# Performance work log

Hardware: AMD Instinct MI355X
Metric: run time of the kernel (lower is better)

The kernel has to match this reference:

```python
import jax, jax.numpy as jnp
import numpy as np

B, N, D, H, DH, FF, L, K, V = 16, 512, 512, 8, 64, 2048, 4, 16, 10000

def _ln(x, g, b, eps=1e-5):
    mu = jnp.mean(x, axis=-1, keepdims=True)
    var = jnp.var(x, axis=-1, keepdims=True)
    return (x - mu) * jax.lax.rsqrt(var + eps) * g + b

def setup_inputs() -> dict:
    key = jax.random.key(0)
    ks = jax.random.split(key, 24)
    s = lambda i, shape, sc=0.02: jax.random.normal(ks[i], shape, dtype=jnp.float32) * sc
    return {
        'node_ids': jax.random.randint(ks[0], (B * N,), 0, V, dtype=jnp.int32),
        'eigvecs': jax.random.normal(ks[1], (B * N, K), dtype=jnp.float32),
        'adj': jax.random.bernoulli(ks[2], 0.1, (B, N, N)),
        'emb': s(3, (V, D), 1.0),
        'pe_w': s(4, (K, D)), 'pe_b': jnp.zeros((D,), jnp.float32),
        'wq': s(5, (L, D, D)), 'bq': jnp.zeros((L, D), jnp.float32),
        'wk': s(6, (L, D, D)), 'bk': jnp.zeros((L, D), jnp.float32),
        'wv': s(7, (L, D, D)), 'bv': jnp.zeros((L, D), jnp.float32),
        'wo': s(8, (L, D, D)), 'bo': jnp.zeros((L, D), jnp.float32),
        'ln1_g': jnp.ones((L, D), jnp.float32), 'ln1_b': jnp.zeros((L, D), jnp.float32),
        'ln2_g': jnp.ones((L, D), jnp.float32), 'ln2_b': jnp.zeros((L, D), jnp.float32),
        'w1': s(9, (L, D, FF)), 'b1': jnp.zeros((L, FF), jnp.float32),
        'w2': s(10, (L, FF, D)), 'b2': jnp.zeros((L, D), jnp.float32),
    }

def reference(node_ids, eigvecs, adj, emb, pe_w, pe_b, wq, bq, wk, bk, wv, bv, wo, bo,
              ln1_g, ln1_b, ln2_g, ln2_b, w1, b1, w2, b2):
    # embedding + Laplacian PE (dropout = identity at eval)
    h = emb[node_ids] + eigvecs @ pe_w + pe_b          # [B*N, D]
    x = h.reshape(B, N, D)                              # dense batch (equal graph sizes)
    # faithful to torch _canonical_mask: -inf WHERE bool mask is True
    mask = jnp.where(adj, -jnp.inf, 0.0)[:, None, :, :]  # [B,1,N,N] broadcast over heads
    scale = 1.0 / jnp.sqrt(jnp.float32(DH))
    for i in range(L):
        q = (x @ wq[i] + bq[i]).reshape(B, N, H, DH)
        k = (x @ wk[i] + bk[i]).reshape(B, N, H, DH)
        v = (x @ wv[i] + bv[i]).reshape(B, N, H, DH)
        scores = jnp.einsum('bqhd,bkhd->bhqk', q, k) * scale + mask
        attn = jax.nn.softmax(scores, axis=-1)
        o = jnp.einsum('bhqk,bkhd->bqhd', attn, v).reshape(B, N, D)
        x = _ln(x + o @ wo[i] + bo[i], ln1_g[i], ln1_b[i])
        ff = jax.nn.relu(x @ w1[i] + b1[i]) @ w2[i] + b2[i]
        x = _ln(x + ff, ln2_g[i], ln2_b[i])
    return x.reshape(B * N, D)  # from_dense_batch with equal graph sizes
```

## Files before the change

### kernel.cpp

```cpp
#include <hip/hip_runtime.h>
#include <math.h>

#define NBATCH 16
#define NSEQ   512
#define DMODEL 512
#define NHEAD  8
#define DHEAD  64
#define FFDIM  2048
#define NLAYER 4
#define MROWS  (NBATCH * NSEQ)

typedef __attribute__((ext_vector_type(8))) short  short8v;
typedef __attribute__((ext_vector_type(4))) float  float4v;
typedef __attribute__((ext_vector_type(4))) unsigned short ushort4v;

__device__ __forceinline__ unsigned short f2bf(float x) {
    unsigned int u = __float_as_uint(x);
    u += 0x7FFFu + ((u >> 16) & 1u);
    return (unsigned short)(u >> 16);
}

__device__ __forceinline__ int xcd_chunk_orig(int bid, int nwg) {
    int q = nwg >> 3;
    return (bid & 7) * q + (bid >> 3);
}

__global__ void zero_flag_kernel(int* flag) {
    if (threadIdx.x == 0 && blockIdx.x == 0) flag[0] = 0;
}
__global__ void detect_adj_kernel(const unsigned char* __restrict__ a, int nbytes,
                                  int* __restrict__ flag) {
    int t = blockIdx.x * blockDim.x + threadIdx.x;
    int i = t * 4 + 1;
    int f = (i < nbytes) && (a[i] != 0);
    if (__any(f)) {
        if ((threadIdx.x & 63) == 0) atomicOr(flag, 1);
    }
}

__global__ __launch_bounds__(256) void build_mask_kernel(
        const void* __restrict__ adjp, const int* __restrict__ flag,
        unsigned long long* __restrict__ Mask) {
    int gw = (blockIdx.x * 256 + threadIdx.x) >> 6;
    int lane = threadIdx.x & 63;
    int nz;
    if (flag[0]) nz = ((const unsigned char*)adjp)[(size_t)gw * 64 + lane] != 0;
    else         nz = ((const int*)adjp)[(size_t)gw * 64 + lane] != 0;
    unsigned long long m = __ballot(nz);
    if (lane == 0) Mask[gw] = m;
}

__global__ __launch_bounds__(256) void transpose_cvt_kernel(
        const float* __restrict__ W, unsigned short* __restrict__ Wt,
        int K, int N, size_t in_stride, size_t out_stride, int row_off) {
    __shared__ float tile[32][33];
    const float* Wl = W + blockIdx.z * in_stride;
    unsigned short* Wo = Wt + blockIdx.z * out_stride;
    int n0 = blockIdx.x * 32, k0 = blockIdx.y * 32;
    int t = threadIdx.x;
    int r = t >> 3, c4 = (t & 7) * 4;
    float4 v = *(const float4*)(Wl + (size_t)(k0 + r) * N + n0 + c4);
    tile[r][c4 + 0] = v.x; tile[r][c4 + 1] = v.y;
    tile[r][c4 + 2] = v.z; tile[r][c4 + 3] = v.w;
    __syncthreads();
    ushort4v o;
    o.x = f2bf(tile[c4 + 0][r]); o.y = f2bf(tile[c4 + 1][r]);
    o.z = f2bf(tile[c4 + 2][r]); o.w = f2bf(tile[c4 + 3][r]);
    *(ushort4v*)(Wo + (size_t)(row_off + n0 + r) * K + k0 + c4) = o;
}

__global__ __launch_bounds__(256) void embed_kernel(
        const int* __restrict__ node_ids, const float* __restrict__ eigvecs,
        const float* __restrict__ emb, const float* __restrict__ pe_w,
        const float* __restrict__ pe_b, float* __restrict__ X,
        unsigned short* __restrict__ Xb) {
    int i = blockIdx.x * 256 + threadIdx.x;
    int row = i >> 9, d = i & 511;
    float acc = emb[(size_t)node_ids[row] * DMODEL + d] + pe_b[d];
    const float* ev = eigvecs + row * 16;
#pragma unroll
    for (int k = 0; k < 16; ++k) acc = fmaf(ev[k], pe_w[k * DMODEL + d], acc);
    X[i] = acc;
    Xb[i] = f2bf(acc);
}

template<int BN, int EPI>
__global__ __launch_bounds__(256) void bgemm_kernel(
        const unsigned short* __restrict__ A, const unsigned short* __restrict__ Bt,
        const float* __restrict__ bias0, const float* __restrict__ bias1,
        const float* __restrict__ bias2, const float* __restrict__ res,
        float* __restrict__ Cf, unsigned short* __restrict__ Cb0,
        unsigned short* __restrict__ Cb1, unsigned short* __restrict__ Cb2,
        int K, int N) {
    constexpr int WM = (BN == 128) ? 2 : 4;
    constexpr int WN = (BN == 128) ? 2 : 1;
    constexpr int MR = 128 / (WM * 16);
    constexpr int NR = BN / (WN * 16);
    __shared__ unsigned short Al[128 * 40];
    __shared__ unsigned short Bl[BN * 40];
    int tid = threadIdx.x;
    int nbn = N / BN;
    int orig = xcd_chunk_orig(blockIdx.x, gridDim.x);
    int bm = orig / nbn;
    int bn = orig - bm * nbn;
    int wid = tid >> 6, lane = tid & 63;
    int wr = wid / WN, wc = wid % WN;
    int l15 = lane & 15, lg = lane >> 4;
    float4v acc[MR][NR];
#pragma unroll
    for (int i = 0; i < MR; ++i)
#pragma unroll
        for (int j = 0; j < NR; ++j) { acc[i][j].x = 0.f; acc[i][j].y = 0.f; acc[i][j].z = 0.f; acc[i][j].w = 0.f; }
    const unsigned short* Ag = A + (size_t)(bm * 128) * K;
    const unsigned short* Bg = Bt + (size_t)(bn * BN) * K;
    for (int k0 = 0; k0 < K; k0 += 32) {
#pragma unroll
        for (int it = 0; it < 2; ++it) {
            int ch = tid + it * 256;
            int row = ch >> 2, c = ch & 3;
            *(short8v*)(Al + row * 40 + c * 8) =
                *(const short8v*)(Ag + (size_t)row * K + k0 + c * 8);
        }
#pragma unroll
        for (int it = 0; it < (BN == 128 ? 2 : 1); ++it) {
            int ch = tid + it * 256;
            int row = ch >> 2, c = ch & 3;
            *(short8v*)(Bl + row * 40 + c * 8) =
                *(const short8v*)(Bg + (size_t)row * K + k0 + c * 8);
        }
        __syncthreads();
        short8v af[MR], bf[NR];
#pragma unroll
        for (int rm = 0; rm < MR; ++rm)
            af[rm] = *(const short8v*)(Al + (wr * MR * 16 + rm * 16 + l15) * 40 + lg * 8);
#pragma unroll
        for (int cn = 0; cn < NR; ++cn)
            bf[cn] = *(const short8v*)(Bl + (wc * NR * 16 + cn * 16 + l15) * 40 + lg * 8);
#pragma unroll
        for (int rm = 0; rm < MR; ++rm)
#pragma unroll
            for (int cn = 0; cn < NR; ++cn)
                acc[rm][cn] = __builtin_amdgcn_mfma_f32_16x16x32_bf16(
                    af[rm], bf[cn], acc[rm][cn], 0, 0, 0);
        __syncthreads();
    }
#pragma unroll
    for (int cn = 0; cn < NR; ++cn) {
        int col = bn * BN + wc * NR * 16 + cn * 16 + l15;
        int seg = col >> 9, cs = col & 511;
        const float* bp = (EPI == 3) ? (seg == 0 ? bias0 : (seg == 1 ? bias1 : bias2)) : bias0;
        unsigned short* op = (EPI == 3) ? (seg == 0 ? Cb0 : (seg == 1 ? Cb1 : Cb2)) : Cb0;
        float bv = bp[(EPI == 3) ? cs : col];
#pragma unroll
        for (int rm = 0; rm < MR; ++rm) {
#pragma unroll
            for (int j = 0; j < 4; ++j) {
                int row = bm * 128 + wr * MR * 16 + rm * 16 + lg * 4 + j;
                float v = acc[rm][cn][j] + bv;
                if (EPI == 1) {
                    v += res[(size_t)row * N + col];
                    Cf[(size_t)row * N + col] = v;
                } else if (EPI == 2) {
                    op[(size_t)row * N + col] = f2bf(fmaxf(v, 0.f));
                } else {
                    op[(size_t)row * 512 + cs] = f2bf(v);
                }
            }
        }
    }
}

__global__ __launch_bounds__(256) void mattn_kernel(
        const unsigned short* __restrict__ Q, const unsigned short* __restrict__ Kb,
        const unsigned short* __restrict__ Vb,
        const unsigned long long* __restrict__ Mask,
        unsigned short* __restrict__ O) {
    __shared__ unsigned short Kl[64 * 72];
    __shared__ unsigned short Vt[64 * 72];
    __shared__ unsigned short Pl[4 * 16 * 72];
    __shared__ unsigned long long Ml[64 * 8];
    int tid = threadIdx.x;
    int bid = xcd_chunk_orig(blockIdx.x, gridDim.x);
    int qb = bid & 7, h = (bid >> 3) & 7, b = bid >> 6;
    int w = tid >> 6, lane = tid & 63, l15 = lane & 15, lg = lane >> 4;
    int q0 = qb * 64 + w * 16;

    {
        int base = (b * NSEQ + qb * 64) * 8;
        for (int it = tid; it < 512; it += 256) Ml[it] = Mask[base + it];
    }
    short8v qf[2];
    {
        const unsigned short* qp = Q + (size_t)(b * NSEQ + q0 + l15) * DMODEL + h * DHEAD + lg * 8;
        qf[0] = *(const short8v*)(qp);
        qf[1] = *(const short8v*)(qp + 32);
    }
    float m[4], lsum[4];
    float4v ao[4];
#pragma unroll
    for (int j = 0; j < 4; ++j) { m[j] = -1e30f; lsum[j] = 0.f; }
#pragma unroll
    for (int cn = 0; cn < 4; ++cn) { ao[cn].x = 0.f; ao[cn].y = 0.f; ao[cn].z = 0.f; ao[cn].w = 0.f; }

    for (int kt = 0; kt < 8; ++kt) {
        int kb0 = kt * 64;
        __syncthreads();
#pragma unroll
        for (int it = 0; it < 2; ++it) {
            int ch = tid + it * 256;
            int row = ch >> 3, c = ch & 7;
            short8v v = *(const short8v*)(Kb + (size_t)(b * NSEQ + kb0 + row) * DMODEL + h * DHEAD + c * 8);
            *(short8v*)(Kl + row * 72 + c * 8) = v;
        }
#pragma unroll
        for (int it = 0; it < 2; ++it) {
            int eb = tid + it * 256;
            int kj = eb & 63, d8 = eb >> 6;
            short8v v = *(const short8v*)(Vb + (size_t)(b * NSEQ + kb0 + kj) * DMODEL + h * DHEAD + d8 * 8);
#pragma unroll
            for (int e = 0; e < 8; ++e)
                Vt[(d8 * 8 + e) * 72 + kj] = (unsigned short)((short*)&v)[e];
        }
        __syncthreads();
        float4v sf[4];
#pragma unroll
        for (int kf = 0; kf < 4; ++kf) {
            short8v k0f = *(const short8v*)(Kl + (kf * 16 + l15) * 72 + lg * 8);
            short8v k1f = *(const short8v*)(Kl + (kf * 16 + l15) * 72 + 32 + lg * 8);
            float4v z; z.x = 0.f; z.y = 0.f; z.z = 0.f; z.w = 0.f;
            z = __builtin_amdgcn_mfma_f32_16x16x32_bf16(qf[0], k0f, z, 0, 0, 0);
            sf[kf] = __builtin_amdgcn_mfma_f32_16x16x32_bf16(qf[1], k1f, z, 0, 0, 0);
        }
        float sv[4][4];
#pragma unroll
        for (int j = 0; j < 4; ++j) {
            unsigned long long wm = Ml[(w * 16 + lg * 4 + j) * 8 + kt];
#pragma unroll
            for (int kf = 0; kf < 4; ++kf) {
                int bit = (int)((wm >> (kf * 16 + l15)) & 1ull);
                sv[kf][j] = sf[kf][j] * 0.125f + (bit ? -1e30f : 0.f);
            }
        }
#pragma unroll
        for (int j = 0; j < 4; ++j) {
            float t = sv[0][j];
#pragma unroll
            for (int kf = 1; kf < 4; ++kf) t = fmaxf(t, sv[kf][j]);
#pragma unroll
            for (int o = 1; o < 16; o <<= 1) t = fmaxf(t, __shfl_xor(t, o));
            float mn = fmaxf(m[j], t);
            float sc = exp2f((m[j] - mn) * 1.44269504f);
            float ps = 0.f;
            int prow = w * 16 + lg * 4 + j;
#pragma unroll
            for (int kf = 0; kf < 4; ++kf) {
                float p = exp2f((sv[kf][j] - mn) * 1.44269504f);
                Pl[prow * 72 + kf * 16 + l15] = f2bf(p);
                ps += p;
            }
#pragma unroll
            for (int o = 1; o < 16; o <<= 1) ps += __shfl_xor(ps, o);
            lsum[j] = lsum[j] * sc + ps;
            m[j] = mn;
#pragma unroll
            for (int cn = 0; cn < 4; ++cn) ao[cn][j] *= sc;
        }
#pragma unroll
        for (int s4 = 0; s4 < 2; ++s4) {
            short8v pa = *(const short8v*)(Pl + (w * 16 + l15) * 72 + s4 * 32 + lg * 8);
#pragma unroll
            for (int cn = 0; cn < 4; ++cn) {
                short8v vbf = *(const short8v*)(Vt + (cn * 16 + l15) * 72 + s4 * 32 + lg * 8);
                ao[cn] = __builtin_amdgcn_mfma_f32_16x16x32_bf16(pa, vbf, ao[cn], 0, 0, 0);
            }
        }
    }
#pragma unroll
    for (int j = 0; j < 4; ++j) lsum[j] = 1.f / lsum[j];
#pragma unroll
    for (int cn = 0; cn < 4; ++cn) {
        int d = cn * 16 + l15;
#pragma unroll
        for (int j = 0; j < 4; ++j) {
            int q = q0 + lg * 4 + j;
            O[(size_t)(b * NSEQ + q) * DMODEL + h * DHEAD + d] = f2bf(ao[cn][j] * lsum[j]);
        }
    }
}

__global__ __launch_bounds__(64) void ln_kernel(
        const float* __restrict__ Xin, const float* __restrict__ g,
        const float* __restrict__ be, float* __restrict__ Y,
        unsigned short* __restrict__ Yb) {
    int row = blockIdx.x;
    int t = threadIdx.x;
    const float* xr = Xin + (size_t)row * DMODEL;
    float4 a = *(const float4*)(xr + (t << 2));
    float4 c = *(const float4*)(xr + 256 + (t << 2));
    float s  = a.x + a.y + a.z + a.w + c.x + c.y + c.z + c.w;
    float ss = a.x*a.x + a.y*a.y + a.z*a.z + a.w*a.w
             + c.x*c.x + c.y*c.y + c.z*c.z + c.w*c.w;
#pragma unroll
    for (int o = 32; o; o >>= 1) { s += __shfl_xor(s, o); ss += __shfl_xor(ss, o); }
    float mu  = s * (1.f / 512.f);
    float var = ss * (1.f / 512.f) - mu * mu;
    float rinv = rsqrtf(var + 1e-5f);
    float4 g0 = *(const float4*)(g + (t << 2));
    float4 g1 = *(const float4*)(g + 256 + (t << 2));
    float4 b0 = *(const float4*)(be + (t << 2));
    float4 b1 = *(const float4*)(be + 256 + (t << 2));
    float4 o0, o1;
    o0.x = (a.x - mu) * rinv * g0.x + b0.x;
    o0.y = (a.y - mu) * rinv * g0.y + b0.y;
    o0.z = (a.z - mu) * rinv * g0.z + b0.z;
    o0.w = (a.w - mu) * rinv * g0.w + b0.w;
    o1.x = (c.x - mu) * rinv * g1.x + b1.x;
    o1.y = (c.y - mu) * rinv * g1.y + b1.y;
    o1.z = (c.z - mu) * rinv * g1.z + b1.z;
    o1.w = (c.w - mu) * rinv * g1.w + b1.w;
    *(float4*)(Y + (size_t)row * DMODEL + (t << 2)) = o0;
    *(float4*)(Y + (size_t)row * DMODEL + 256 + (t << 2)) = o1;
    if (Yb) {
        ushort4v u0, u1;
        u0.x = f2bf(o0.x); u0.y = f2bf(o0.y); u0.z = f2bf(o0.z); u0.w = f2bf(o0.w);
        u1.x = f2bf(o1.x); u1.y = f2bf(o1.y); u1.z = f2bf(o1.z); u1.w = f2bf(o1.w);
        *(ushort4v*)(Yb + (size_t)row * DMODEL + (t << 2)) = u0;
        *(ushort4v*)(Yb + (size_t)row * DMODEL + 256 + (t << 2)) = u1;
    }
}

extern "C" void kernel_launch(void* const* d_in, const int* in_sizes, int n_in,
                              void* d_out, int out_size, void* d_ws, size_t ws_size,
                              hipStream_t stream) {
    const int*   node_ids = (const int*)d_in[0];
    const float* eigvecs  = (const float*)d_in[1];
    const void*  adj      = d_in[2];
    const float* emb      = (const float*)d_in[3];
    const float* pe_w     = (const float*)d_in[4];
    const float* pe_b     = (const float*)d_in[5];
    const float* wq = (const float*)d_in[6];
    const float* bq = (const float*)d_in[7];
    const float* wk = (const float*)d_in[8];
    const float* bk = (const float*)d_in[9];
    const float* wv = (const float*)d_in[10];
    const float* bv = (const float*)d_in[11];
    const float* wo = (const float*)d_in[12];
    const float* bo = (const float*)d_in[13];
    const float* ln1_g = (const float*)d_in[14];
    const float* ln1_b = (const float*)d_in[15];
    const float* ln2_g = (const float*)d_in[16];
    const float* ln2_b = (const float*)d_in[17];
    const float* w1 = (const float*)d_in[18];
    const float* b1 = (const float*)d_in[19];
    const float* w2 = (const float*)d_in[20];
    const float* b2 = (const float*)d_in[21];
    float* out = (float*)d_out;

    const size_t MB = 1024ull * 1024ull;
    char* ws = (char*)d_ws;
    float*          X  = (float*)(ws + 0 * MB);
    float*          T  = (float*)(ws + 16 * MB);
    unsigned short* Xb = (unsigned short*)(ws + 32 * MB);
    unsigned short* Qb = (unsigned short*)(ws + 40 * MB);
    unsigned short* Kc = (unsigned short*)(ws + 48 * MB);
    unsigned short* Vc = (unsigned short*)(ws + 56 * MB);
    unsigned short* Ob = (unsigned short*)(ws + 64 * MB);
    unsigned short* Fb = (unsigned short*)(ws + 72 * MB);
    unsigned short* wqkvt = (unsigned short*)(ws + 104 * MB);
    unsigned short* wot   = (unsigned short*)(ws + 110 * MB);
    unsigned short* w1t   = (unsigned short*)(ws + 112 * MB);
    unsigned short* w2t   = (unsigned short*)(ws + 120 * MB);
    unsigned long long* Mask = (unsigned long long*)(ws + 128 * MB);
    int*            flag = (int*)(ws + 129 * MB);
    if (ws_size < 130 * MB) return;

    const size_t DD = (size_t)DMODEL * DMODEL;
    const size_t DF = (size_t)DMODEL * FFDIM;
    const size_t QKV = (size_t)3 * DD;

    zero_flag_kernel<<<1, 64, 0, stream>>>(flag);
    detect_adj_kernel<<<4096, 256, 0, stream>>>((const unsigned char*)adj,
                                                NBATCH * NSEQ * NSEQ, flag);
    build_mask_kernel<<<(MROWS * 8 * 64) / 256, 256, 0, stream>>>(adj, flag, Mask);
    {
        dim3 gdd(DMODEL / 32, DMODEL / 32, NLAYER);
        transpose_cvt_kernel<<<gdd, 256, 0, stream>>>(wq, wqkvt, DMODEL, DMODEL, DD, QKV, 0);
        transpose_cvt_kernel<<<gdd, 256, 0, stream>>>(wk, wqkvt, DMODEL, DMODEL, DD, QKV, 512);
        transpose_cvt_kernel<<<gdd, 256, 0, stream>>>(wv, wqkvt, DMODEL, DMODEL, DD, QKV, 1024);
        transpose_cvt_kernel<<<gdd, 256, 0, stream>>>(wo, wot, DMODEL, DMODEL, DD, DD, 0);
        dim3 g1t(FFDIM / 32, DMODEL / 32, NLAYER);
        transpose_cvt_kernel<<<g1t, 256, 0, stream>>>(w1, w1t, DMODEL, FFDIM, DF, DF, 0);
        dim3 g2t(DMODEL / 32, FFDIM / 32, NLAYER);
        transpose_cvt_kernel<<<g2t, 256, 0, stream>>>(w2, w2t, FFDIM, DMODEL, DF, DF, 0);
    }
    embed_kernel<<<(MROWS * DMODEL) / 256, 256, 0, stream>>>(node_ids, eigvecs, emb,
                                                             pe_w, pe_b, X, Xb);
    const int gQKV = (1536 / 128) * (MROWS / 128);
    const int gF   = (FFDIM / 128) * (MROWS / 128);
    const int gO   = (DMODEL / 64) * (MROWS / 128);
    const int gA   = NBATCH * NHEAD * (NSEQ / 64);
    for (int i = 0; i < NLAYER; ++i) {
        bgemm_kernel<128, 3><<<gQKV, 256, 0, stream>>>(
            Xb, wqkvt + i * QKV, bq + i * DMODEL, bk + i * DMODEL, bv + i * DMODEL,
            nullptr, nullptr, Qb, Kc, Vc, DMODEL, 1536);
        mattn_kernel<<<gA, 256, 0, stream>>>(
            Qb, Kc, Vc, Mask, Ob);
        bgemm_kernel<64, 1><<<gO, 256, 0, stream>>>(
            Ob, wot + i * DD, bo + i * DMODEL, nullptr, nullptr,
            X, T, nullptr, nullptr, nullptr, DMODEL, DMODEL);
        ln_kernel<<<MROWS, 64, 0, stream>>>(T, ln1_g + i * DMODEL, ln1_b + i * DMODEL, X, Xb);
        bgemm_kernel<128, 2><<<gF, 256, 0, stream>>>(
            Xb, w1t + i * DF, b1 + i * FFDIM, nullptr, nullptr,
            nullptr, nullptr, Fb, nullptr, nullptr, DMODEL, FFDIM);
        bgemm_kernel<64, 1><<<gO, 256, 0, stream>>>(
            Fb, w2t + i * DF, b2 + i * DMODEL, nullptr, nullptr,
            X, T, nullptr, nullptr, nullptr, FFDIM, DMODEL);
        int last = (i == NLAYER - 1);
        ln_kernel<<<MROWS, 64, 0, stream>>>(T, ln2_g + i * DMODEL, ln2_b + i * DMODEL,
                                            last ? out : X, last ? nullptr : Xb);
    }
}
```

Measured before the change: 899.2 us.

## Double-buffer GEMM tiles using direct global-to-LDS loads

The bf16 GEMM kernel now stages its A and B tiles with global_load_lds, which writes straight into LDS without passing through registers. It also uses two LDS buffers so the next K-slice is fetched while the current one feeds the MFMAs. The goal is to hide global memory latency and cut register traffic in the main loop. The unpadded 32-element row stride can cause LDS bank conflicts on the fragment reads. Correctness depends on the loop's synchronisation also waiting for the asynchronous LDS writes to finish.

```diff
diff --git a/kernel.cpp b/kernel.cpp
--- a/kernel.cpp
+++ b/kernel.cpp
@@ -18,6 +18,12 @@
     unsigned int u = __float_as_uint(x);
     u += 0x7FFFu + ((u >> 16) & 1u);
     return (unsigned short)(u >> 16);
+}
+
+__device__ __forceinline__ void gload16(const unsigned short* g, unsigned short* l) {
+    __builtin_amdgcn_global_load_lds(
+        (const __attribute__((address_space(1))) unsigned int*)g,
+        (__attribute__((address_space(3))) unsigned int*)l, 16, 0, 0);
 }
 
 __device__ __forceinline__ int xcd_chunk_orig(int bid, int nwg) {
@@ -96,8 +102,9 @@
     constexpr int WN = (BN == 128) ? 2 : 1;
     constexpr int MR = 128 / (WM * 16);
     constexpr int NR = BN / (WN * 16);
-    __shared__ unsigned short Al[128 * 40];
-    __shared__ unsigned short Bl[BN * 40];
+    constexpr int BCH = BN / 64;
+    __shared__ unsigned short Al[2][128 * 32];
+    __shared__ unsigned short Bl[2][BN * 32];
     int tid = threadIdx.x;
     int nbn = N / BN;
     int orig = xcd_chunk_orig(blockIdx.x, gridDim.x);
@@ -113,29 +120,35 @@
         for (int j = 0; j < NR; ++j) { acc[i][j].x = 0.f; acc[i][j].y = 0.f; acc[i][j].z = 0.f; acc[i][j].w = 0.f; }
     const unsigned short* Ag = A + (size_t)(bm * 128) * K;
     const unsigned short* Bg = Bt + (size_t)(bn * BN) * K;
-    for (int k0 = 0; k0 < K; k0 += 32) {
+
+    auto STAGE = [&](int buf, int k0) {
 #pragma unroll
         for (int it = 0; it < 2; ++it) {
-            int ch = tid + it * 256;
+            int ch = it * 256 + tid;
             int row = ch >> 2, c = ch & 3;
-            *(short8v*)(Al + row * 40 + c * 8) =
-                *(const short8v*)(Ag + (size_t)row * K + k0 + c * 8);
-        }
-#pragma unroll
-        for (int it = 0; it < (BN == 128 ? 2 : 1); ++it) {
-            int ch = tid + it * 256;
+            gload16(Ag + (size_t)row * K + k0 + c * 8, &Al[buf][ch * 8]);
+        }
+#pragma unroll
+        for (int it = 0; it < BCH; ++it) {
+            int ch = it * 256 + tid;
             int row = ch >> 2, c = ch & 3;
-            *(short8v*)(Bl + row * 40 + c * 8) =
-                *(const short8v*)(Bg + (size_t)row * K + k0 + c * 8);
-        }
-        __syncthreads();
+            gload16(Bg + (size_t)row * K + k0 + c * 8, &Bl[buf][ch * 8]);
+        }
+    };
+
+    STAGE(0, 0);
+    __syncthreads();
+    int nt = K >> 5;
+    for (int t = 0; t < nt; ++t) {
+        int cur = t & 1;
+        if (t + 1 < nt) STAGE(cur ^ 1, (t + 1) << 5);
         short8v af[MR], bf[NR];
 #pragma unroll
         for (int rm = 0; rm < MR; ++rm)
-            af[rm] = *(const short8v*)(Al + (wr * MR * 16 + rm * 16 + l15) * 40 + lg * 8);
+            af[rm] = *(const short8v*)(&Al[cur][(wr * MR * 16 + rm * 16 + l15) * 32 + lg * 8]);
 #pragma unroll
         for (int cn = 0; cn < NR; ++cn)
-            bf[cn] = *(const short8v*)(Bl + (wc * NR * 16 + cn * 16 + l15) * 40 + lg * 8);
+            bf[cn] = *(const short8v*)(&Bl[cur][(wc * NR * 16 + cn * 16 + l15) * 32 + lg * 8]);
 #pragma unroll
         for (int rm = 0; rm < MR; ++rm)
 #pragma unroll
```

After: 858.5 us. 4.5% less time.
